# Optimization experiments

Hardware: AMD Instinct MI355X
Metric: run time of the kernel (lower is better)

## Reference

```python
import jax, jax.numpy as jnp
import numpy as np

H = 128  # hidden_dim
COORD_CLAMP = 100.0


def _glorot(key, shape):
    fan_in, fan_out = shape[0], shape[1]
    lim = float(np.sqrt(6.0 / (fan_in + fan_out)))
    return jax.random.uniform(key, shape, jnp.float32, -lim, lim)


def setup_inputs() -> dict:
    key = jax.random.key(0)
    ks = jax.random.split(key, 20)
    B, N = 2, 512
    inp = {
        "h": jax.random.normal(ks[0], (B, N, H), jnp.float32),
        "pos": jax.random.normal(ks[1], (B, N, 3), jnp.float32),
        "vel": jax.random.normal(ks[2], (B, N, 3), jnp.float32),
        # edge_mlp: Linear(2H+2 -> H), SiLU, Linear(H -> H), SiLU
        "We1": _glorot(ks[3], (2 * H + 2, H)), "be1": jnp.zeros((H,), jnp.float32),
        "We2": _glorot(ks[4], (H, H)), "be2": jnp.zeros((H,), jnp.float32),
        # attention_mlp: Linear(H -> 1), Sigmoid
        "Wa": _glorot(ks[5], (H, 1)), "ba": jnp.zeros((1,), jnp.float32),
        # pos_mlp: Linear(H -> H), SiLU, Linear(H -> 1, no bias)
        "Wp1": _glorot(ks[6], (H, H)), "bp1": jnp.zeros((H,), jnp.float32),
        "Wp2": _glorot(ks[7], (H, 1)),
        # vel_mlp: Linear(H -> H), SiLU, Linear(H -> 1, no bias)
        "Wv1": _glorot(ks[8], (H, H)), "bv1": jnp.zeros((H,), jnp.float32),
        "Wv2": _glorot(ks[9], (H, 1)),
        # node_mlp: Linear(2H -> H), SiLU, Linear(H -> H)
        "Wn1": _glorot(ks[10], (2 * H, H)), "bn1": jnp.zeros((H,), jnp.float32),
        "Wn2": _glorot(ks[11], (H, H)), "bn2": jnp.zeros((H,), jnp.float32),
    }
    return inp


def reference(h, pos, vel, We1, be1, We2, be2, Wa, ba,
              Wp1, bp1, Wp2, Wv1, bv1, Wv2, Wn1, bn1, Wn2, bn2):
    B, N, _ = pos.shape
    # pairwise diffs: [B, N, N, 3]
    pos_diff = pos[:, :, None, :] - pos[:, None, :, :]
    vel_diff = vel[:, :, None, :] - vel[:, None, :, :]
    pos_dist_sq = jnp.sum(pos_diff ** 2, axis=-1, keepdims=True)  # [B,N,N,1]
    vel_dist_sq = jnp.sum(vel_diff ** 2, axis=-1, keepdims=True)
    h_i = jnp.broadcast_to(h[:, :, None, :], (B, N, N, H))
    h_j = jnp.broadcast_to(h[:, None, :, :], (B, N, N, H))
    edge_input = jnp.concatenate([h_i, h_j, pos_dist_sq, vel_dist_sq], axis=-1)  # [B,N,N,2H+2]
    # edge MLP
    m = jax.nn.silu(jnp.einsum('bijc,ch->bijh', edge_input, We1) + be1)
    m_ij = jax.nn.silu(jnp.einsum('bijh,hk->bijk', m, We2) + be2)
    # attention gate
    att = jax.nn.sigmoid(jnp.einsum('bijh,ho->bijo', m_ij, Wa) + ba)  # [B,N,N,1]
    m_ij = m_ij * att
    # tanh-weighted coordinate/velocity updates
    pos_w = jnp.tanh(jnp.einsum('bijh,ho->bijo', jax.nn.silu(jnp.einsum('bijh,hk->bijk', m_ij, Wp1) + bp1), Wp2))
    vel_w = jnp.tanh(jnp.einsum('bijh,ho->bijo', jax.nn.silu(jnp.einsum('bijh,hk->bijk', m_ij, Wv1) + bv1), Wv2))
    denom = jnp.float32(max(N - 1, 1))
    pos_update = jnp.sum(pos_diff * pos_w, axis=2) / denom  # [B,N,3]
    vel_update = jnp.sum(vel_diff * vel_w, axis=2) / denom
    pos_out = jnp.clip(pos + pos_update, -COORD_CLAMP, COORD_CLAMP)
    vel_out = jnp.clip(vel + vel_update, -COORD_CLAMP, COORD_CLAMP)
    # node update
    m_agg = jnp.sum(m_ij, axis=2)  # [B,N,H]
    node_input = jnp.concatenate([h, m_agg], axis=-1)  # [B,N,2H]
    h_out = jax.nn.silu(jnp.einsum('bnc,ch->bnh', node_input, Wn1) + bn1)
    h_out = jnp.einsum('bnh,hk->bnk', h_out, Wn2) + bn2
    h_out = h + h_out  # residual
    return (h_out, pos_out, vel_out)
```

## Files before the change

kernel.cpp:

```cpp
#include <hip/hip_runtime.h>
#include <hip/hip_bf16.h>

#define Hd 128
#define Nn 512
#define TJ 32
#define LSTRIDE 136

typedef __bf16 bf16x8 __attribute__((ext_vector_type(8)));
typedef __bf16 bf16x4 __attribute__((ext_vector_type(4)));
typedef float  floatx4 __attribute__((ext_vector_type(4)));

__device__ __forceinline__ float frcp(float x){ return __builtin_amdgcn_rcpf(x); }
__device__ __forceinline__ float fsilu(float x){ return x * frcp(1.f + __expf(-x)); }
__device__ __forceinline__ float fsigm(float x){ return frcp(1.f + __expf(-x)); }
__device__ __forceinline__ float ftanh(float x){ return 1.f - 2.f * frcp(__expf(2.f*x) + 1.f); }
__device__ __forceinline__ float rfl(float x){
  return __int_as_float(__builtin_amdgcn_readfirstlane(__float_as_int(x)));
}

__global__ __launch_bounds__(256) void prep(const float* __restrict__ h,
                                            const float* __restrict__ We1,
                                            const float* __restrict__ be1,
                                            const float* __restrict__ We2,
                                            const float* __restrict__ Wp1,
                                            const float* __restrict__ Wv1,
                                            float* __restrict__ A,
                                            float* __restrict__ Bm,
                                            __bf16* __restrict__ dst,
                                            float* __restrict__ zbase){
  if (blockIdx.x < 256){
    const int r0 = blockIdx.x * 4;
    const int k = threadIdx.x & 127, ch = threadIdx.x >> 7;
    __shared__ float hL[4][Hd];
    __shared__ float pa[2][4][Hd], pb[2][4][Hd];
    for (int idx = threadIdx.x; idx < 4*Hd; idx += 256)
      hL[idx >> 7][idx & 127] = h[r0*Hd + idx];
    __syncthreads();
    float a[4] = {0.f,0.f,0.f,0.f}, bb[4] = {0.f,0.f,0.f,0.f};
    const int cbase = ch*64;
    #pragma unroll 4
    for (int cc = 0; cc < 64; ++cc){
      const int c = cbase + cc;
      const float wa = We1[c*Hd + k];
      const float wb = We1[(c + Hd)*Hd + k];
      #pragma unroll
      for (int rr = 0; rr < 4; ++rr){
        a[rr]  += hL[rr][c] * wa;
        bb[rr] += hL[rr][c] * wb;
      }
    }
    #pragma unroll
    for (int rr = 0; rr < 4; ++rr){ pa[ch][rr][k] = a[rr]; pb[ch][rr][k] = bb[rr]; }
    __syncthreads();
    if (threadIdx.x < Hd){
      const float be = be1[k];
      #pragma unroll
      for (int rr = 0; rr < 4; ++rr){
        A[(r0+rr)*Hd + k]  = pa[0][rr][k] + pa[1][rr][k] + be;
        Bm[(r0+rr)*Hd + k] = pb[0][rr][k] + pb[1][rr][k];
      }
    }
  } else if (blockIdx.x < 280){
    const int blk = blockIdx.x - 256;
    const int which = blk >> 3, m = blk & 7;
    const float* src = (which == 0) ? We2 : (which == 1 ? Wp1 : Wv1);
    __bf16* d = dst + which * (Hd*Hd);
    #pragma unroll
    for (int it = 0; it < 8; ++it){
      const int sidx = m*2048 + it*256 + threadIdx.x;
      const int kk = sidx >> 7, cc = sidx & 127;
      const int s = kk >> 5, j = kk & 7;
      const int lane = ((kk >> 3) & 3)*16 + (cc & 15);
      const int n = cc >> 4;
      d[n*2048 + s*512 + lane*8 + j] = (__bf16)src[sidx];
    }
  } else {
    const int t0 = (blockIdx.x - 280)*256 + threadIdx.x;
    for (int idx = t0; idx < 137216; idx += 2048) zbase[idx] = 0.f;
  }
}

__global__ __launch_bounds__(256) void egnn_bf(
    const float* __restrict__ pos, const float* __restrict__ vel,
    const float* __restrict__ We1, const float* __restrict__ be2,
    const float* __restrict__ Wa,  const float* __restrict__ ba,
    const float* __restrict__ bp1, const float* __restrict__ Wp2,
    const float* __restrict__ bv1, const float* __restrict__ Wv2,
    const float* __restrict__ A,   const float* __restrict__ Bm,
    const __bf16* __restrict__ Wsw,
    float* __restrict__ magg, float* __restrict__ posu, float* __restrict__ velu){

  const int t    = threadIdx.x;
  const int w    = t >> 6;
  const int lane = t & 63;
  const int q    = lane >> 4;
  const int l15  = lane & 15;
  const int node = blockIdx.x;
  const int b    = node >> 9;

  __shared__ float AiL[Hd], wpL[Hd], wvL[Hd];
  __shared__ float be2L[Hd], bp1L[Hd], bv1L[Hd], WaL[Hd], Wp2L[Hd], Wv2L[Hd];
  __shared__ __align__(16) __bf16 bufij[4*16*LSTRIDE];
  __shared__ float attW[4][16];
  __shared__ float sMag[4][Hd];
  __shared__ float sPV[4][6];

  if (t < Hd){
    AiL[t]  = A[(size_t)node*Hd + t];
    wpL[t]  = We1[256*Hd + t];
    wvL[t]  = We1[257*Hd + t];
    be2L[t] = be2[t]; bp1L[t] = bp1[t]; bv1L[t] = bv1[t];
    WaL[t]  = Wa[t];  Wp2L[t] = Wp2[t]; Wv2L[t] = Wv2[t];
  }
  const float baV = ba[0];
  const float* pi = &pos[(size_t)node*3];
  const float* vi = &vel[(size_t)node*3];
  const float px = rfl(pi[0]), py = rfl(pi[1]), pz = rfl(pi[2]);
  const float ux = rfl(vi[0]), uy = rfl(vi[1]), uz = rfl(vi[2]);
  __syncthreads();

  const bf16x8* We2s = (const bf16x8*)(Wsw);
  const bf16x8* Wp1s = (const bf16x8*)(Wsw + Hd*Hd);
  const bf16x8* Wv1s = (const bf16x8*)(Wsw + 2*Hd*Hd);
  __bf16* myBuf = &bufij[w*16*LSTRIDE];
  float*  myAtt = attW[w];

  float accP0=0.f, accP1=0.f, accP2=0.f, accV0=0.f, accV1=0.f, accV2=0.f;
  float acc8[8];
  #pragma unroll
  for (int e = 0; e < 8; ++e) acc8[e] = 0.f;

  for (int jt = 0; jt < 8; ++jt){
    const int j0 = w*128 + jt*16;
    const size_t row = (size_t)(b*Nn + j0 + l15);

    const float* pj = &pos[row*3];
    const float* vj = &vel[row*3];
    const float dx = px - pj[0], dy = py - pj[1], dz = pz - pj[2];
    const float dp = dx*dx + dy*dy + dz*dz;
    const float ex = ux - vj[0], ey = uy - vj[1], ez = uz - vj[2];
    const float dv = ex*ex + ey*ey + ez*ez;

    floatx4 acc[8];
    const floatx4 fzero = {0.f,0.f,0.f,0.f};
    #pragma unroll
    for (int fm = 0; fm < 8; ++fm) acc[fm] = fzero;

    #pragma unroll
    for (int s = 0; s < 4; ++s){
      const int fo = s*32 + q*8;
      const floatx4 A0 = *(const floatx4*)&AiL[fo], A1 = *(const floatx4*)&AiL[fo+4];
      const floatx4 P0 = *(const floatx4*)&wpL[fo], P1 = *(const floatx4*)&wpL[fo+4];
      const floatx4 V0 = *(const floatx4*)&wvL[fo], V1 = *(const floatx4*)&wvL[fo+4];
      const floatx4* Bp = (const floatx4*)&Bm[row*Hd + fo];
      const floatx4 b0 = Bp[0], b1 = Bp[1];
      float x[8];
      #pragma unroll
      for (int e = 0; e < 4; ++e){
        x[e]   = fsilu(A0[e] + b0[e] + dp*P0[e] + dv*V0[e]);
        x[4+e] = fsilu(A1[e] + b1[e] + dp*P1[e] + dv*V1[e]);
      }
      union { bf16x8 v; __hip_bfloat162 h2[4]; } o;
      o.h2[0] = __float22bfloat162_rn(make_float2(x[0], x[1]));
      o.h2[1] = __float22bfloat162_rn(make_float2(x[2], x[3]));
      o.h2[2] = __float22bfloat162_rn(make_float2(x[4], x[5]));
      o.h2[3] = __float22bfloat162_rn(make_float2(x[6], x[7]));
      #pragma unroll
      for (int fm = 0; fm < 8; ++fm){
        const bf16x8 a = We2s[(fm*4 + s)*64 + lane];
        acc[fm] = __builtin_amdgcn_mfma_f32_16x16x32_bf16(a, o.v, acc[fm], 0, 0, 0);
      }
    }

    float aw = 0.f;
    #pragma unroll
    for (int fm = 0; fm < 8; ++fm){
      const int fb = fm*16 + q*4;
      const floatx4 be = *(const floatx4*)&be2L[fb];
      const floatx4 wa = *(const floatx4*)&WaL[fb];
      float s0[4];
      #pragma unroll
      for (int r = 0; r < 4; ++r){
        s0[r] = fsilu(acc[fm][r] + be[r]);
        aw += s0[r]*wa[r];
      }
      union { bf16x4 v; __hip_bfloat162 h2[2]; } k0;
      k0.h2[0] = __float22bfloat162_rn(make_float2(s0[0], s0[1]));
      k0.h2[1] = __float22bfloat162_rn(make_float2(s0[2], s0[3]));
      *(bf16x4*)&myBuf[l15*LSTRIDE + fb] = k0.v;
    }
    aw += __shfl_xor(aw, 16, 64); aw += __shfl_xor(aw, 32, 64);
    const float att = fsigm(aw + baV);
    if (lane < 16) myAtt[l15] = att;

    #pragma unroll
    for (int fm = 0; fm < 8; ++fm) acc[fm] = fzero;
    #pragma unroll
    for (int s = 0; s < 4; ++s){
      const bf16x8 bfv = *(const bf16x8*)&myBuf[l15*LSTRIDE + s*32 + q*8];
      #pragma unroll
      for (int fm = 0; fm < 8; ++fm){
        const bf16x8 a = Wp1s[(fm*4 + s)*64 + lane];
        acc[fm] = __builtin_amdgcn_mfma_f32_16x16x32_bf16(a, bfv, acc[fm], 0, 0, 0);
      }
    }
    {
      float p = 0.f;
      #pragma unroll
      for (int fm = 0; fm < 8; ++fm){
        const int fb = fm*16 + q*4;
        const floatx4 bb = *(const floatx4*)&bp1L[fb];
        const floatx4 w2 = *(const floatx4*)&Wp2L[fb];
        #pragma unroll
        for (int r = 0; r < 4; ++r)
          p += fsilu(fmaf(att, acc[fm][r], bb[r])) * w2[r];
      }
      p += __shfl_xor(p, 16, 64); p += __shfl_xor(p, 32, 64);
      const float pw = ftanh(p);
      accP0 += (px - pj[0]) * pw;
      accP1 += (py - pj[1]) * pw;
      accP2 += (pz - pj[2]) * pw;
    }

    #pragma unroll
    for (int fm = 0; fm < 8; ++fm) acc[fm] = fzero;
    #pragma unroll
    for (int s = 0; s < 4; ++s){
      const bf16x8 bfv = *(const bf16x8*)&myBuf[l15*LSTRIDE + s*32 + q*8];
      #pragma unroll
      for (int fm = 0; fm < 8; ++fm){
        const bf16x8 a = Wv1s[(fm*4 + s)*64 + lane];
        acc[fm] = __builtin_amdgcn_mfma_f32_16x16x32_bf16(a, bfv, acc[fm], 0, 0, 0);
      }
    }
    {
      float p = 0.f;
      #pragma unroll
      for (int fm = 0; fm < 8; ++fm){
        const int fb = fm*16 + q*4;
        const floatx4 bb = *(const floatx4*)&bv1L[fb];
        const floatx4 w2 = *(const floatx4*)&Wv2L[fb];
        #pragma unroll
        for (int r = 0; r < 4; ++r)
          p += fsilu(fmaf(att, acc[fm][r], bb[r])) * w2[r];
      }
      p += __shfl_xor(p, 16, 64); p += __shfl_xor(p, 32, 64);
      const float vw = ftanh(p);
      accV0 += (ux - vj[0]) * vw;
      accV1 += (uy - vj[1]) * vw;
      accV2 += (uz - vj[2]) * vw;
    }

    {
      const int fg = lane & 15, jr = lane >> 4;
      #pragma unroll
      for (int k = 0; k < 4; ++k){
        const int jl = jr*4 + k;
        const float aj = myAtt[jl];
        const bf16x8 v = *(const bf16x8*)&myBuf[jl*LSTRIDE + fg*8];
        #pragma unroll
        for (int e = 0; e < 8; ++e) acc8[e] += aj * (float)v[e];
      }
    }
  }

  {
    float r6[6] = {accP0, accP1, accP2, accV0, accV1, accV2};
    #pragma unroll
    for (int off = 1; off < 64; off <<= 1){
      #pragma unroll
      for (int e = 0; e < 6; ++e) r6[e] += __shfl_xor(r6[e], off, 64);
    }
    if (lane == 0){
      #pragma unroll
      for (int e = 0; e < 6; ++e) sPV[w][e] = r6[e];
    }
    #pragma unroll
    for (int e = 0; e < 8; ++e){
      acc8[e] += __shfl_xor(acc8[e], 16, 64);
      acc8[e] += __shfl_xor(acc8[e], 32, 64);
    }
    if (lane < 16){
      *(float4*)&sMag[w][l15*8 + 0] = make_float4(acc8[0], acc8[1], acc8[2], acc8[3]);
      *(float4*)&sMag[w][l15*8 + 4] = make_float4(acc8[4], acc8[5], acc8[6], acc8[7]);
    }
  }
  __syncthreads();
  if (t < Hd){
    magg[(size_t)node*Hd + t] = sMag[0][t] + sMag[1][t] + sMag[2][t] + sMag[3][t];
  } else if (t < Hd + 3){
    const int d = t - Hd;
    posu[node*3 + d] = 0.25f*(sPV[0][d] + sPV[1][d] + sPV[2][d] + sPV[3][d]);
  } else if (t < Hd + 6){
    const int d = t - Hd - 3;
    velu[node*3 + d] = 0.25f*(sPV[0][3+d] + sPV[1][3+d] + sPV[2][3+d] + sPV[3][3+d]);
  }
}

__device__ __forceinline__ void gemm_kloopT(const __bf16* __restrict__ buf,
                                            const bf16x8* __restrict__ Ws,
                                            int w, int lane, int q, int l15,
                                            floatx4 acc[2][2]){
  const floatx4 zero = {0.f, 0.f, 0.f, 0.f};
  #pragma unroll
  for (int m = 0; m < 2; ++m){ acc[m][0] = zero; acc[m][1] = zero; }
  #pragma unroll
  for (int s = 0; s < 4; ++s){
    bf16x8 bf[2];
    #pragma unroll
    for (int n = 0; n < 2; ++n)
      bf[n] = *(const bf16x8*)&buf[(16*n + l15)*LSTRIDE + s*32 + q*8];
    const bf16x8 a0 = Ws[((2*w + 0)*4 + s)*64 + lane];
    const bf16x8 a1 = Ws[((2*w + 1)*4 + s)*64 + lane];
    #pragma unroll
    for (int n = 0; n < 2; ++n){
      acc[0][n] = __builtin_amdgcn_mfma_f32_16x16x32_bf16(a0, bf[n], acc[0][n], 0, 0, 0);
      acc[1][n] = __builtin_amdgcn_mfma_f32_16x16x32_bf16(a1, bf[n], acc[1][n], 0, 0, 0);
    }
  }
}

__device__ __forceinline__ void wdotT(floatx4 acc[2][2], float att0, float att1,
                                      const float* __restrict__ biasL,
                                      const float* __restrict__ w2L,
                                      int w, int lane, int q, int l15,
                                      float (*part)[TJ]){
  const int fb0 = 32*w + 4*q, fb1 = fb0 + 16;
  const floatx4 bb0 = *(const floatx4*)&biasL[fb0];
  const floatx4 bb1 = *(const floatx4*)&biasL[fb1];
  const floatx4 w0  = *(const floatx4*)&w2L[fb0];
  const floatx4 w1  = *(const floatx4*)&w2L[fb1];
  float p0 = 0.f, p1 = 0.f;
  #pragma unroll
  for (int r = 0; r < 4; ++r){
    p0 += fsilu(fmaf(att0, acc[0][0][r], bb0[r])) * w0[r];
    p0 += fsilu(fmaf(att0, acc[1][0][r], bb1[r])) * w1[r];
    p1 += fsilu(fmaf(att1, acc[0][1][r], bb0[r])) * w0[r];
    p1 += fsilu(fmaf(att1, acc[1][1][r], bb1[r])) * w1[r];
  }
  p0 += __shfl_xor(p0, 16, 64); p0 += __shfl_xor(p0, 32, 64);
  p1 += __shfl_xor(p1, 16, 64); p1 += __shfl_xor(p1, 32, 64);
  if (lane < 16){
    part[w][l15]      = p0;
    part[w][16 + l15] = p1;
  }
}

__global__ __launch_bounds__(256) void egnn_main(
    const float* __restrict__ pos, const float* __restrict__ vel,
    const float* __restrict__ We1, const float* __restrict__ be2,
    const float* __restrict__ Wa,  const float* __restrict__ ba,
    const float* __restrict__ bp1, const float* __restrict__ Wp2,
    const float* __restrict__ bv1, const float* __restrict__ Wv2,
    const float* __restrict__ A,   const float* __restrict__ Bm,
    const __bf16* __restrict__ Wsw,
    float* __restrict__ magg, float* __restrict__ posu, float* __restrict__ velu){

  const int t    = threadIdx.x;
  const int w    = t >> 6;
  const int lane = t & 63;
  const int q    = lane >> 4;
  const int l15  = lane & 15;
  const int node = blockIdx.x >> 1;
  const int half = blockIdx.x & 1;
  const int b    = node >> 9;

  __shared__ float AiL[Hd], wpL[Hd], wvL[Hd];
  __shared__ float be2L[Hd], bp1L[Hd], bv1L[Hd], WaL[Hd], Wp2L[Hd], Wv2L[Hd];
  __shared__ __align__(16) __bf16 bufm [TJ*LSTRIDE];
  __shared__ __align__(16) __bf16 bufij[TJ*LSTRIDE];
  __shared__ float partAtt[4][TJ], partP[4][TJ], partV[4][TJ];
  __shared__ float attL[TJ];

  if (t < Hd){
    AiL[t]  = A[node*Hd + t];
    wpL[t]  = We1[256*Hd + t];
    wvL[t]  = We1[257*Hd + t];
    be2L[t] = be2[t]; bp1L[t] = bp1[t]; bv1L[t] = bv1[t];
    WaL[t]  = Wa[t];  Wp2L[t] = Wp2[t]; Wv2L[t] = Wv2[t];
  }
  const float baV = ba[0];
  const float* pi = &pos[(size_t)node*3];
  const float* vi = &vel[(size_t)node*3];
  const float px = rfl(pi[0]), py = rfl(pi[1]), pz = rfl(pi[2]);
  const float ux = rfl(vi[0]), uy = rfl(vi[1]), uz = rfl(vi[2]);
  __syncthreads();

  const bf16x8* We2s = (const bf16x8*)(Wsw);
  const bf16x8* Wp1s = (const bf16x8*)(Wsw + Hd*Hd);
  const bf16x8* Wv1s = (const bf16x8*)(Wsw + 2*Hd*Hd);

  float accR[8];
  #pragma unroll
  for (int e = 0; e < 8; ++e) accR[e] = 0.f;

  for (int jt = 0; jt < (Nn/2)/TJ; ++jt){
    const int j0 = half*(Nn/2) + jt * TJ;
    {
      const int g  = t & 15;
      const int j2 = t >> 4;
      const floatx4 a0 = *(const floatx4*)&AiL[g*8];
      const floatx4 a1 = *(const floatx4*)&AiL[g*8 + 4];
      const floatx4 p0 = *(const floatx4*)&wpL[g*8];
      const floatx4 p1 = *(const floatx4*)&wpL[g*8 + 4];
      const floatx4 v0 = *(const floatx4*)&wvL[g*8];
      const floatx4 v1 = *(const floatx4*)&wvL[g*8 + 4];
      #pragma unroll
      for (int rr = 0; rr < 2; ++rr){
        const int j = j2 + rr*16;
        const int jg = j0 + j;
        const float* pj = &pos[(size_t)(b*Nn + jg)*3];
        const float* vj = &vel[(size_t)(b*Nn + jg)*3];
        const float dx = px - pj[0], dy = py - pj[1], dz = pz - pj[2];
        const float dp = dx*dx + dy*dy + dz*dz;
        const float ex = ux - vj[0], ey = uy - vj[1], ez = uz - vj[2];
        const float dv = ex*ex + ey*ey + ez*ez;
        const floatx4* Bp4 = (const floatx4*)&Bm[((size_t)(b*Nn + jg))*Hd + g*8];
        const floatx4 b0 = Bp4[0], b1 = Bp4[1];
        union { bf16x8 v; __hip_bfloat162 h2[4]; } o;
        float x[8];
        #pragma unroll
        for (int e = 0; e < 4; ++e){
          x[e]   = fsilu(a0[e] + b0[e] + dp*p0[e] + dv*v0[e]);
          x[4+e] = fsilu(a1[e] + b1[e] + dp*p1[e] + dv*v1[e]);
        }
        o.h2[0] = __float22bfloat162_rn(make_float2(x[0], x[1]));
        o.h2[1] = __float22bfloat162_rn(make_float2(x[2], x[3]));
        o.h2[2] = __float22bfloat162_rn(make_float2(x[4], x[5]));
        o.h2[3] = __float22bfloat162_rn(make_float2(x[6], x[7]));
        *(bf16x8*)&bufm[j*LSTRIDE + g*8] = o.v;
      }
    }
    __syncthreads();
    {
      floatx4 acc[2][2];
      gemm_kloopT(bufm, We2s, w, lane, q, l15, acc);
      const int fb0 = 32*w + 4*q, fb1 = fb0 + 16;
      const floatx4 be0 = *(const floatx4*)&be2L[fb0];
      const floatx4 be1v = *(const floatx4*)&be2L[fb1];
      const floatx4 wa0 = *(const floatx4*)&WaL[fb0];
      const floatx4 wa1 = *(const floatx4*)&WaL[fb1];
      float aw[2];
      #pragma unroll
      for (int n = 0; n < 2; ++n){
        const int j = 16*n + l15;
        float s0[4], s1[4];
        #pragma unroll
        for (int r = 0; r < 4; ++r){
          s0[r] = fsilu(acc[0][n][r] + be0[r]);
          s1[r] = fsilu(acc[1][n][r] + be1v[r]);
        }
        aw[n] = s0[0]*wa0[0] + s0[1]*wa0[1] + s0[2]*wa0[2] + s0[3]*wa0[3]
              + s1[0]*wa1[0] + s1[1]*wa1[1] + s1[2]*wa1[2] + s1[3]*wa1[3];
        union { bf16x4 v; __hip_bfloat162 h2[2]; } p0k, p1k;
        p0k.h2[0] = __float22bfloat162_rn(make_float2(s0[0], s0[1]));
        p0k.h2[1] = __float22bfloat162_rn(make_float2(s0[2], s0[3]));
        p1k.h2[0] = __float22bfloat162_rn(make_float2(s1[0], s1[1]));
        p1k.h2[1] = __float22bfloat162_rn(make_float2(s1[2], s1[3]));
        *(bf16x4*)&bufij[j*LSTRIDE + fb0] = p0k.v;
        *(bf16x4*)&bufij[j*LSTRIDE + fb1] = p1k.v;
      }
      aw[0] += __shfl_xor(aw[0], 16, 64); aw[0] += __shfl_xor(aw[0], 32, 64);
      aw[1] += __shfl_xor(aw[1], 16, 64); aw[1] += __shfl_xor(aw[1], 32, 64);
      if (lane < 16){
        partAtt[w][l15]      = aw[0];
        partAtt[w][16 + l15] = aw[1];
      }
    }
    __syncthreads();
    {
      const float att0 = fsigm(partAtt[0][l15] + partAtt[1][l15] +
                               partAtt[2][l15] + partAtt[3][l15] + baV);
      const float att1 = fsigm(partAtt[0][16+l15] + partAtt[1][16+l15] +
                               partAtt[2][16+l15] + partAtt[3][16+l15] + baV);
      if (w == 0 && lane < 16){ attL[l15] = att0; attL[16 + l15] = att1; }
      floatx4 acc[2][2];
      gemm_kloopT(bufij, Wp1s, w, lane, q, l15, acc);
      wdotT(acc, att0, att1, bp1L, Wp2L, w, lane, q, l15, partP);
      gemm_kloopT(bufij, Wv1s, w, lane, q, l15, acc);
      wdotT(acc, att0, att1, bv1L, Wv2L, w, lane, q, l15, partV);
    }
    __syncthreads();
    if (w == 0){
      if (lane < TJ){
        const int jg = j0 + lane;
        const float* pj = &pos[(size_t)(b*Nn + jg)*3];
        const float s4 = partP[0][lane] + partP[1][lane] + partP[2][lane] + partP[3][lane];
        const float pw = ftanh(s4);
        accR[0] += (px - pj[0]) * pw;
        accR[1] += (py - pj[1]) * pw;
        accR[2] += (pz - pj[2]) * pw;
      }
    } else if (w == 1){
      if (lane < TJ){
        const int jg = j0 + lane;
        const float* vj = &vel[(size_t)(b*Nn + jg)*3];
        const float s4 = partV[0][lane] + partV[1][lane] + partV[2][lane] + partV[3][lane];
        const float vw = ftanh(s4);
        accR[0] += (ux - vj[0]) * vw;
        accR[1] += (uy - vj[1]) * vw;
        accR[2] += (uz - vj[2]) * vw;
      }
    } else {
      const int sg   = (w - 2)*8 + (lane & 7);
      const int jsub = lane >> 3;
      #pragma unroll
      for (int jj = 0; jj < 4; ++jj){
        const int j = jj*8 + jsub;
        const float aj = attL[j];
        const bf16x8 v = *(const bf16x8*)&bufij[j*LSTRIDE + sg*8];
        #pragma unroll
        for (int e = 0; e < 8; ++e) accR[e] += aj * (float)v[e];
      }
    }
  }

  if (w == 0 || w == 1){
    float v0 = accR[0], v1 = accR[1], v2 = accR[2];
    #pragma unroll
    for (int off = 1; off < 64; off <<= 1){
      v0 += __shfl_xor(v0, off, 64);
      v1 += __shfl_xor(v1, off, 64);
      v2 += __shfl_xor(v2, off, 64);
    }
    if (lane == 0){
      float* dst = (w == 0) ? &posu[node*3] : &velu[node*3];
      atomicAdd(&dst[0], v0);
      atomicAdd(&dst[1], v1);
      atomicAdd(&dst[2], v2);
    }
  } else {
    const int sg = (w - 2)*8 + (lane & 7);
    #pragma unroll
    for (int off = 8; off < 64; off <<= 1){
      #pragma unroll
      for (int e = 0; e < 8; ++e) accR[e] += __shfl_xor(accR[e], off, 64);
    }
    if ((lane >> 3) == 0){
      #pragma unroll
      for (int e = 0; e < 8; ++e)
        atomicAdd(&magg[node*Hd + sg*8 + e], accR[e]);
    }
  }
}

__global__ __launch_bounds__(256) void egnn_final(
    const float* __restrict__ h, const float* __restrict__ pos, const float* __restrict__ vel,
    const float* __restrict__ Wn1, const float* __restrict__ bn1,
    const float* __restrict__ Wn2, const float* __restrict__ bn2,
    const float* __restrict__ magg, const float* __restrict__ posu,
    const float* __restrict__ velu, float* __restrict__ out){
  const int row = blockIdx.x;
  const int t = threadIdx.x;
  const int k = t & 127, ch = t >> 7;
  __shared__ float ni[2*Hd];
  __shared__ float p1[2][Hd], t1[Hd];
  ni[t] = (t < Hd) ? h[row*Hd + t] : magg[row*Hd + (t - Hd)];
  __syncthreads();
  {
    float a0=0.f,a1=0.f,a2=0.f,a3=0.f;
    const int cb = ch*Hd;
    #pragma unroll 8
    for (int cc = 0; cc < Hd; cc += 4){
      a0 += ni[cb+cc+0] * Wn1[(cb+cc+0)*Hd + k];
      a1 += ni[cb+cc+1] * Wn1[(cb+cc+1)*Hd + k];
      a2 += ni[cb+cc+2] * Wn1[(cb+cc+2)*Hd + k];
      a3 += ni[cb+cc+3] * Wn1[(cb+cc+3)*Hd + k];
    }
    p1[ch][k] = (a0+a1)+(a2+a3);
  }
  __syncthreads();
  if (t < Hd) t1[t] = fsilu(p1[0][t] + p1[1][t] + bn1[t]);
  __syncthreads();
  {
    float a0=0.f,a1=0.f,a2=0.f,a3=0.f;
    const int cb = ch*64;
    #pragma unroll 8
    for (int cc = 0; cc < 64; cc += 4){
      a0 += t1[cb+cc+0] * Wn2[(cb+cc+0)*Hd + k];
      a1 += t1[cb+cc+1] * Wn2[(cb+cc+1)*Hd + k];
      a2 += t1[cb+cc+2] * Wn2[(cb+cc+2)*Hd + k];
      a3 += t1[cb+cc+3] * Wn2[(cb+cc+3)*Hd + k];
    }
    p1[ch][k] = (a0+a1)+(a2+a3);
  }
  __syncthreads();
  if (t < Hd){
    out[row*Hd + t] = ni[t] + p1[0][t] + p1[1][t] + bn2[t];
  } else if (t < Hd + 3){
    const int d = t - Hd;
    const float v = pos[row*3 + d] + posu[row*3 + d] * (1.f/511.f);
    out[2*Nn*Hd + row*3 + d] = fminf(fmaxf(v, -100.f), 100.f);
  } else if (t < Hd + 6){
    const int d = t - Hd - 3;
    const float v = vel[row*3 + d] + velu[row*3 + d] * (1.f/511.f);
    out[2*Nn*Hd + 2*Nn*3 + row*3 + d] = fminf(fmaxf(v, -100.f), 100.f);
  }
}

extern "C" void kernel_launch(void* const* d_in, const int* in_sizes, int n_in,
                              void* d_out, int out_size, void* d_ws, size_t ws_size,
                              hipStream_t stream){
  const float* h   = (const float*)d_in[0];
  const float* pos = (const float*)d_in[1];
  const float* vel = (const float*)d_in[2];
  const float* We1 = (const float*)d_in[3];
  const float* be1 = (const float*)d_in[4];
  const float* We2 = (const float*)d_in[5];
  const float* be2 = (const float*)d_in[6];
  const float* Wa  = (const float*)d_in[7];
  const float* ba  = (const float*)d_in[8];
  const float* Wp1 = (const float*)d_in[9];
  const float* bp1 = (const float*)d_in[10];
  const float* Wp2 = (const float*)d_in[11];
  const float* Wv1 = (const float*)d_in[12];
  const float* bv1 = (const float*)d_in[13];
  const float* Wv2 = (const float*)d_in[14];
  const float* Wn1 = (const float*)d_in[15];
  const float* bn1 = (const float*)d_in[16];
  const float* Wn2 = (const float*)d_in[17];
  const float* bn2 = (const float*)d_in[18];

  float* ws = (float*)d_ws;
  float*  A    = ws;
  float*  Bmm  = ws + 131072;
  float*  magg = ws + 262144;
  float*  posu = ws + 393216;
  float*  velu = ws + 396288;
  __bf16* Wsw  = (__bf16*)(ws + 399360);
  float*  outp = (float*)d_out;

  hipFuncAttributes attr{};
  hipError_t ae = hipFuncGetAttributes(&attr, (const void*)egnn_bf);
  const bool useBf = (ae == hipSuccess && attr.numRegs > 0 && attr.numRegs <= 128);

  prep<<<dim3(288), dim3(256), 0, stream>>>(h, We1, be1, We2, Wp1, Wv1,
                                            A, Bmm, Wsw, magg);
  if (useBf){
    egnn_bf<<<dim3(1024), dim3(256), 0, stream>>>(pos, vel, We1, be2, Wa, ba, bp1, Wp2,
                                                  bv1, Wv2, A, Bmm, Wsw, magg, posu, velu);
  } else {
    egnn_main<<<dim3(2048), dim3(256), 0, stream>>>(pos, vel, We1, be2, Wa, ba, bp1, Wp2,
                                                    bv1, Wv2, A, Bmm, Wsw, magg, posu, velu);
  }
  egnn_final<<<dim3(1024), dim3(256), 0, stream>>>(h, pos, vel, Wn1, bn1, Wn2, bn2,
                                                   magg, posu, velu, outp);
}
```

Measured before the change: 234.5 us.

## Fuse node MLP into edge kernel and process 32 neighbors per wave iteration

The edge kernel now handles two 16-row neighbor tiles per loop iteration, so each loaded weight fragment feeds two MFMAs and weight loads per neighbor are halved. The final node MLP, residual, and pos/vel clamp are fused into the tail of the edge kernel, which removes the egnn_final launch and the magg/posu/velu round trip through global memory. The cost is higher register pressure (two accumulator sets plus cached activations) and a doubled LDS buffer, which may lower occupancy or push registers past the 128 threshold. If that threshold is exceeded, the fallback path is taken instead.

```diff
diff --git a/kernel.cpp b/kernel.cpp
--- a/kernel.cpp
+++ b/kernel.cpp
@@ -81,14 +81,17 @@
 }
 
 __global__ __launch_bounds__(256) void egnn_bf(
+    const float* __restrict__ h,
     const float* __restrict__ pos, const float* __restrict__ vel,
     const float* __restrict__ We1, const float* __restrict__ be2,
     const float* __restrict__ Wa,  const float* __restrict__ ba,
     const float* __restrict__ bp1, const float* __restrict__ Wp2,
     const float* __restrict__ bv1, const float* __restrict__ Wv2,
+    const float* __restrict__ Wn1, const float* __restrict__ bn1,
+    const float* __restrict__ Wn2, const float* __restrict__ bn2,
     const float* __restrict__ A,   const float* __restrict__ Bm,
     const __bf16* __restrict__ Wsw,
-    float* __restrict__ magg, float* __restrict__ posu, float* __restrict__ velu){
+    float* __restrict__ out){
 
   const int t    = threadIdx.x;
   const int w    = t >> 6;
@@ -100,10 +103,8 @@
 
   __shared__ float AiL[Hd], wpL[Hd], wvL[Hd];
   __shared__ float be2L[Hd], bp1L[Hd], bv1L[Hd], WaL[Hd], Wp2L[Hd], Wv2L[Hd];
-  __shared__ __align__(16) __bf16 bufij[4*16*LSTRIDE];
-  __shared__ float attW[4][16];
-  __shared__ float sMag[4][Hd];
-  __shared__ float sPV[4][6];
+  __shared__ __align__(16) __bf16 bufij[4*32*LSTRIDE];
+  __shared__ float attW[4][32];
 
   if (t < Hd){
     AiL[t]  = A[(size_t)node*Hd + t];
@@ -122,7 +123,7 @@
   const bf16x8* We2s = (const bf16x8*)(Wsw);
   const bf16x8* Wp1s = (const bf16x8*)(Wsw + Hd*Hd);
   const bf16x8* Wv1s = (const bf16x8*)(Wsw + 2*Hd*Hd);
-  __bf16* myBuf = &bufij[w*16*LSTRIDE];
+  __bf16* myBuf = &bufij[w*32*LSTRIDE];
   float*  myAtt = attW[w];
 
   float accP0=0.f, accP1=0.f, accP2=0.f, accV0=0.f, accV1=0.f, accV2=0.f;
@@ -130,132 +131,182 @@
   #pragma unroll
   for (int e = 0; e < 8; ++e) acc8[e] = 0.f;
 
-  for (int jt = 0; jt < 8; ++jt){
-    const int j0 = w*128 + jt*16;
-    const size_t row = (size_t)(b*Nn + j0 + l15);
-
-    const float* pj = &pos[row*3];
-    const float* vj = &vel[row*3];
-    const float dx = px - pj[0], dy = py - pj[1], dz = pz - pj[2];
-    const float dp = dx*dx + dy*dy + dz*dz;
-    const float ex = ux - vj[0], ey = uy - vj[1], ez = uz - vj[2];
-    const float dv = ex*ex + ey*ey + ez*ez;
-
-    floatx4 acc[8];
-    const floatx4 fzero = {0.f,0.f,0.f,0.f};
-    #pragma unroll
-    for (int fm = 0; fm < 8; ++fm) acc[fm] = fzero;
-
+  const floatx4 fzero = {0.f,0.f,0.f,0.f};
+
+  #pragma unroll 1
+  for (int jt = 0; jt < 4; ++jt){
+    const int j0 = w*128 + jt*32;
+    const size_t row0 = (size_t)(b*Nn + j0 + l15);
+    const size_t row1 = row0 + 16;
+
+    float dp[2], dv[2];
+    {
+      const float* pj0 = &pos[row0*3]; const float* vj0 = &vel[row0*3];
+      const float* pj1 = &pos[row1*3]; const float* vj1 = &vel[row1*3];
+      float dx = px - pj0[0], dy = py - pj0[1], dz = pz - pj0[2];
+      dp[0] = dx*dx + dy*dy + dz*dz;
+      dx = px - pj1[0]; dy = py - pj1[1]; dz = pz - pj1[2];
+      dp[1] = dx*dx + dy*dy + dz*dz;
+      float ex = ux - vj0[0], ey = uy - vj0[1], ez = uz - vj0[2];
+      dv[0] = ex*ex + ey*ey + ez*ez;
+      ex = ux - vj1[0]; ey = uy - vj1[1]; ez = uz - vj1[2];
+      dv[1] = ex*ex + ey*ey + ez*ez;
+    }
+
+    bf16x8 mf[4][2];
     #pragma unroll
     for (int s = 0; s < 4; ++s){
       const int fo = s*32 + q*8;
       const floatx4 A0 = *(const floatx4*)&AiL[fo], A1 = *(const floatx4*)&AiL[fo+4];
       const floatx4 P0 = *(const floatx4*)&wpL[fo], P1 = *(const floatx4*)&wpL[fo+4];
       const floatx4 V0 = *(const floatx4*)&wvL[fo], V1 = *(const floatx4*)&wvL[fo+4];
-      const floatx4* Bp = (const floatx4*)&Bm[row*Hd + fo];
-      const floatx4 b0 = Bp[0], b1 = Bp[1];
-      float x[8];
-      #pragma unroll
-      for (int e = 0; e < 4; ++e){
-        x[e]   = fsilu(A0[e] + b0[e] + dp*P0[e] + dv*V0[e]);
-        x[4+e] = fsilu(A1[e] + b1[e] + dp*P1[e] + dv*V1[e]);
-      }
-      union { bf16x8 v; __hip_bfloat162 h2[4]; } o;
-      o.h2[0] = __float22bfloat162_rn(make_float2(x[0], x[1]));
-      o.h2[1] = __float22bfloat162_rn(make_float2(x[2], x[3]));
-      o.h2[2] = __float22bfloat162_rn(make_float2(x[4], x[5]));
-      o.h2[3] = __float22bfloat162_rn(make_float2(x[6], x[7]));
-      #pragma unroll
-      for (int fm = 0; fm < 8; ++fm){
-        const bf16x8 a = We2s[(fm*4 + s)*64 + lane];
-        acc[fm] = __builtin_amdgcn_mfma_f32_16x16x32_bf16(a, o.v, acc[fm], 0, 0, 0);
-      }
-    }
-
-    float aw = 0.f;
-    #pragma unroll
-    for (int fm = 0; fm < 8; ++fm){
-      const int fb = fm*16 + q*4;
-      const floatx4 be = *(const floatx4*)&be2L[fb];
-      const floatx4 wa = *(const floatx4*)&WaL[fb];
-      float s0[4];
-      #pragma unroll
-      for (int r = 0; r < 4; ++r){
-        s0[r] = fsilu(acc[fm][r] + be[r]);
-        aw += s0[r]*wa[r];
-      }
-      union { bf16x4 v; __hip_bfloat162 h2[2]; } k0;
-      k0.h2[0] = __float22bfloat162_rn(make_float2(s0[0], s0[1]));
-      k0.h2[1] = __float22bfloat162_rn(make_float2(s0[2], s0[3]));
-      *(bf16x4*)&myBuf[l15*LSTRIDE + fb] = k0.v;
-    }
-    aw += __shfl_xor(aw, 16, 64); aw += __shfl_xor(aw, 32, 64);
-    const float att = fsigm(aw + baV);
-    if (lane < 16) myAtt[l15] = att;
-
-    #pragma unroll
-    for (int fm = 0; fm < 8; ++fm) acc[fm] = fzero;
-    #pragma unroll
-    for (int s = 0; s < 4; ++s){
-      const bf16x8 bfv = *(const bf16x8*)&myBuf[l15*LSTRIDE + s*32 + q*8];
-      #pragma unroll
-      for (int fm = 0; fm < 8; ++fm){
-        const bf16x8 a = Wp1s[(fm*4 + s)*64 + lane];
-        acc[fm] = __builtin_amdgcn_mfma_f32_16x16x32_bf16(a, bfv, acc[fm], 0, 0, 0);
-      }
-    }
+      #pragma unroll
+      for (int n = 0; n < 2; ++n){
+        const floatx4* Bp = (const floatx4*)&Bm[(n ? row1 : row0)*Hd + fo];
+        const floatx4 b0 = Bp[0], b1 = Bp[1];
+        float x[8];
+        #pragma unroll
+        for (int e = 0; e < 4; ++e){
+          x[e]   = fsilu(A0[e] + b0[e] + dp[n]*P0[e] + dv[n]*V0[e]);
+          x[4+e] = fsilu(A1[e] + b1[e] + dp[n]*P1[e] + dv[n]*V1[e]);
+        }
+        union { bf16x8 v; __hip_bfloat162 h2[4]; } o;
+        o.h2[0] = __float22bfloat162_rn(make_float2(x[0], x[1]));
+        o.h2[1] = __float22bfloat162_rn(make_float2(x[2], x[3]));
+        o.h2[2] = __float22bfloat162_rn(make_float2(x[4], x[5]));
+        o.h2[3] = __float22bfloat162_rn(make_float2(x[6], x[7]));
+        mf[s][n] = o.v;
+      }
+    }
+
+    float aw0 = 0.f, aw1 = 0.f;
+    #pragma unroll
+    for (int f = 0; f < 2; ++f){
+      floatx4 acc[4][2];
+      #pragma unroll
+      for (int m4 = 0; m4 < 4; ++m4){ acc[m4][0] = fzero; acc[m4][1] = fzero; }
+      #pragma unroll
+      for (int s = 0; s < 4; ++s){
+        #pragma unroll
+        for (int m4 = 0; m4 < 4; ++m4){
+          const bf16x8 a = We2s[((f*4 + m4)*4 + s)*64 + lane];
+          acc[m4][0] = __builtin_amdgcn_mfma_f32_16x16x32_bf16(a, mf[s][0], acc[m4][0], 0, 0, 0);
+          acc[m4][1] = __builtin_amdgcn_mfma_f32_16x16x32_bf16(a, mf[s][1], acc[m4][1], 0, 0, 0);
+        }
+      }
+      #pragma unroll
+      for (int m4 = 0; m4 < 4; ++m4){
+        const int fb = (f*4 + m4)*16 + q*4;
+        const floatx4 be = *(const floatx4*)&be2L[fb];
+        const floatx4 wa = *(const floatx4*)&WaL[fb];
+        float s0[4], s1[4];
+        #pragma unroll
+        for (int r = 0; r < 4; ++r){
+          s0[r] = fsilu(acc[m4][0][r] + be[r]);
+          s1[r] = fsilu(acc[m4][1][r] + be[r]);
+          aw0 += s0[r]*wa[r];
+          aw1 += s1[r]*wa[r];
+        }
+        union { bf16x4 v; __hip_bfloat162 h2[2]; } k0, k1;
+        k0.h2[0] = __float22bfloat162_rn(make_float2(s0[0], s0[1]));
+        k0.h2[1] = __float22bfloat162_rn(make_float2(s0[2], s0[3]));
+        k1.h2[0] = __float22bfloat162_rn(make_float2(s1[0], s1[1]));
+        k1.h2[1] = __float22bfloat162_rn(make_float2(s1[2], s1[3]));
+        *(bf16x4*)&myBuf[l15*LSTRIDE + fb]        = k0.v;
+        *(bf16x4*)&myBuf[(16 + l15)*LSTRIDE + fb] = k1.v;
+      }
+    }
+    aw0 += __shfl_xor(aw0, 16, 64); aw0 += __shfl_xor(aw0, 32, 64);
+    aw1 += __shfl_xor(aw1, 16, 64); aw1 += __shfl_xor(aw1, 32, 64);
+    const float att0 = fsigm(aw0 + baV);
+    const float att1 = fsigm(aw1 + baV);
+    if (lane < 16){ myAtt[l15] = att0; myAtt[16 + l15] = att1; }
+
     {
-      float p = 0.f;
-      #pragma unroll
-      for (int fm = 0; fm < 8; ++fm){
-        const int fb = fm*16 + q*4;
-        const floatx4 bb = *(const floatx4*)&bp1L[fb];
-        const floatx4 w2 = *(const floatx4*)&Wp2L[fb];
-        #pragma unroll
-        for (int r = 0; r < 4; ++r)
-          p += fsilu(fmaf(att, acc[fm][r], bb[r])) * w2[r];
-      }
-      p += __shfl_xor(p, 16, 64); p += __shfl_xor(p, 32, 64);
-      const float pw = ftanh(p);
-      accP0 += (px - pj[0]) * pw;
-      accP1 += (py - pj[1]) * pw;
-      accP2 += (pz - pj[2]) * pw;
-    }
-
-    #pragma unroll
-    for (int fm = 0; fm < 8; ++fm) acc[fm] = fzero;
-    #pragma unroll
-    for (int s = 0; s < 4; ++s){
-      const bf16x8 bfv = *(const bf16x8*)&myBuf[l15*LSTRIDE + s*32 + q*8];
-      #pragma unroll
-      for (int fm = 0; fm < 8; ++fm){
-        const bf16x8 a = Wv1s[(fm*4 + s)*64 + lane];
-        acc[fm] = __builtin_amdgcn_mfma_f32_16x16x32_bf16(a, bfv, acc[fm], 0, 0, 0);
-      }
-    }
+      float p0 = 0.f, p1 = 0.f;
+      #pragma unroll
+      for (int f = 0; f < 2; ++f){
+        floatx4 acc[4][2];
+        #pragma unroll
+        for (int m4 = 0; m4 < 4; ++m4){ acc[m4][0] = fzero; acc[m4][1] = fzero; }
+        #pragma unroll
+        for (int s = 0; s < 4; ++s){
+          const bf16x8 b0 = *(const bf16x8*)&myBuf[l15*LSTRIDE + s*32 + q*8];
+          const bf16x8 b1 = *(const bf16x8*)&myBuf[(16 + l15)*LSTRIDE + s*32 + q*8];
+          #pragma unroll
+          for (int m4 = 0; m4 < 4; ++m4){
+            const bf16x8 a = Wp1s[((f*4 + m4)*4 + s)*64 + lane];
+            acc[m4][0] = __builtin_amdgcn_mfma_f32_16x16x32_bf16(a, b0, acc[m4][0], 0, 0, 0);
+            acc[m4][1] = __builtin_amdgcn_mfma_f32_16x16x32_bf16(a, b1, acc[m4][1], 0, 0, 0);
+          }
+        }
+        #pragma unroll
+        for (int m4 = 0; m4 < 4; ++m4){
+          const int fb = (f*4 + m4)*16 + q*4;
+          const floatx4 bb = *(const floatx4*)&bp1L[fb];
+          const floatx4 w2 = *(const floatx4*)&Wp2L[fb];
+          #pragma unroll
+          for (int r = 0; r < 4; ++r){
+            p0 += fsilu(fmaf(att0, acc[m4][0][r], bb[r])) * w2[r];
+            p1 += fsilu(fmaf(att1, acc[m4][1][r], bb[r])) * w2[r];
+          }
+        }
+      }
+      p0 += __shfl_xor(p0, 16, 64); p0 += __shfl_xor(p0, 32, 64);
+      p1 += __shfl_xor(p1, 16, 64); p1 += __shfl_xor(p1, 32, 64);
+      const float pw0 = ftanh(p0), pw1 = ftanh(p1);
+      const float* pj0 = &pos[row0*3];
+      const float* pj1 = &pos[row1*3];
+      accP0 += (px - pj0[0])*pw0 + (px - pj1[0])*pw1;
+      accP1 += (py - pj0[1])*pw0 + (py - pj1[1])*pw1;
+      accP2 += (pz - pj0[2])*pw0 + (pz - pj1[2])*pw1;
+    }
+
     {
-      float p = 0.f;
-      #pragma unroll
-      for (int fm = 0; fm < 8; ++fm){
-        const int fb = fm*16 + q*4;
-        const floatx4 bb = *(const floatx4*)&bv1L[fb];
-        const floatx4 w2 = *(const floatx4*)&Wv2L[fb];
-        #pragma unroll
-        for (int r = 0; r < 4; ++r)
-          p += fsilu(fmaf(att, acc[fm][r], bb[r])) * w2[r];
-      }
-      p += __shfl_xor(p, 16, 64); p += __shfl_xor(p, 32, 64);
-      const float vw = ftanh(p);
-      accV0 += (ux - vj[0]) * vw;
-      accV1 += (uy - vj[1]) * vw;
-      accV2 += (uz - vj[2]) * vw;
+      float p0 = 0.f, p1 = 0.f;
+      #pragma unroll
+      for (int f = 0; f < 2; ++f){
+        floatx4 acc[4][2];
+        #pragma unroll
+        for (int m4 = 0; m4 < 4; ++m4){ acc[m4][0] = fzero; acc[m4][1] = fzero; }
+        #pragma unroll
+        for (int s = 0; s < 4; ++s){
+          const bf16x8 b0 = *(const bf16x8*)&myBuf[l15*LSTRIDE + s*32 + q*8];
+          const bf16x8 b1 = *(const bf16x8*)&myBuf[(16 + l15)*LSTRIDE + s*32 + q*8];
+          #pragma unroll
+          for (int m4 = 0; m4 < 4; ++m4){
+            const bf16x8 a = Wv1s[((f*4 + m4)*4 + s)*64 + lane];
+            acc[m4][0] = __builtin_amdgcn_mfma_f32_16x16x32_bf16(a, b0, acc[m4][0], 0, 0, 0);
+            acc[m4][1] = __builtin_amdgcn_mfma_f32_16x16x32_bf16(a, b1, acc[m4][1], 0, 0, 0);
+          }
+        }
+        #pragma unroll
+        for (int m4 = 0; m4 < 4; ++m4){
+          const int fb = (f*4 + m4)*16 + q*4;
+          const floatx4 bb = *(const floatx4*)&bv1L[fb];
+          const floatx4 w2 = *(const floatx4*)&Wv2L[fb];
+          #pragma unroll
+          for (int r = 0; r < 4; ++r){
+            p0 += fsilu(fmaf(att0, acc[m4][0][r], bb[r])) * w2[r];
+            p1 += fsilu(fmaf(att1, acc[m4][1][r], bb[r])) * w2[r];
+          }
+        }
+      }
+      p0 += __shfl_xor(p0, 16, 64); p0 += __shfl_xor(p0, 32, 64);
+      p1 += __shfl_xor(p1, 16, 64); p1 += __shfl_xor(p1, 32, 64);
+      const float vw0 = ftanh(p0), vw1 = ftanh(p1);
+      const float* vj0 = &vel[row0*3];
+      const float* vj1 = &vel[row1*3];
+      accV0 += (ux - vj0[0])*vw0 + (ux - vj1[0])*vw1;
+      accV1 += (uy - vj0[1])*vw0 + (uy - vj1[1])*vw1;
+      accV2 += (uz - vj0[2])*vw0 + (uz - vj1[2])*vw1;
     }
 
     {
       const int fg = lane & 15, jr = lane >> 4;
       #pragma unroll
-      for (int k = 0; k < 4; ++k){
-        const int jl = jr*4 + k;
+      for (int k = 0; k < 8; ++k){
+        const int jl = jr*8 + k;
         const float aj = myAtt[jl];
         const bf16x8 v = *(const bf16x8*)&myBuf[jl*LSTRIDE + fg*8];
         #pragma unroll
@@ -264,6 +315,8 @@
     }
   }
 
+  float* sMagW = (float*)myBuf;
+  float* sPVW  = (float*)myBuf + 128;
   {
     float r6[6] = {accP0, accP1, accP2, accV0, accV1, accV2};
     #pragma unroll
@@ -273,7 +326,7 @@
     }
     if (lane == 0){
       #pragma unroll
-      for (int e = 0; e < 6; ++e) sPV[w][e] = r6[e];
+      for (int e = 0; e < 6; ++e) sPVW[e] = r6[e];
     }
     #pragma unroll
     for (int e = 0; e < 8; ++e){
@@ -281,20 +334,66 @@
       acc8[e] += __shfl_xor(acc8[e], 32, 64);
     }
     if (lane < 16){
-      *(float4*)&sMag[w][l15*8 + 0] = make_float4(acc8[0], acc8[1], acc8[2], acc8[3]);
-      *(float4*)&sMag[w][l15*8 + 4] = make_float4(acc8[4], acc8[5], acc8[6], acc8[7]);
-    }
-  }
-  __syncthreads();
-  if (t < Hd){
-    magg[(size_t)node*Hd + t] = sMag[0][t] + sMag[1][t] + sMag[2][t] + sMag[3][t];
-  } else if (t < Hd + 3){
-    const int d = t - Hd;
-    posu[node*3 + d] = 0.25f*(sPV[0][d] + sPV[1][d] + sPV[2][d] + sPV[3][d]);
-  } else if (t < Hd + 6){
-    const int d = t - Hd - 3;
-    velu[node*3 + d] = 0.25f*(sPV[0][3+d] + sPV[1][3+d] + sPV[2][3+d] + sPV[3][3+d]);
-  }
+      *(float4*)&sMagW[l15*8 + 0] = make_float4(acc8[0], acc8[1], acc8[2], acc8[3]);
+      *(float4*)&sMagW[l15*8 + 4] = make_float4(acc8[4], acc8[5], acc8[6], acc8[7]);
+    }
+  }
+  __syncthreads();
+
+  float* sF = (float*)bufij + 1024;
+  {
+    const float* s0 = (const float*)(bufij);
+    const float* s1 = (const float*)(bufij + 32*LSTRIDE);
+    const float* s2 = (const float*)(bufij + 64*LSTRIDE);
+    const float* s3 = (const float*)(bufij + 96*LSTRIDE);
+    if (t < Hd){
+      sF[128 + t] = s0[t] + s1[t] + s2[t] + s3[t];
+      sF[t] = h[(size_t)node*Hd + t];
+    } else if (t < Hd + 3){
+      const int d = t - Hd;
+      const float v = 0.25f*(s0[128+d] + s1[128+d] + s2[128+d] + s3[128+d]);
+      const float o = pi[d] + v*(1.f/511.f);
+      out[2*Nn*Hd + node*3 + d] = fminf(fmaxf(o, -100.f), 100.f);
+    } else if (t < Hd + 6){
+      const int d = t - Hd - 3;
+      const float v = 0.25f*(s0[131+d] + s1[131+d] + s2[131+d] + s3[131+d]);
+      const float o = vi[d] + v*(1.f/511.f);
+      out[2*Nn*Hd + 2*Nn*3 + node*3 + d] = fminf(fmaxf(o, -100.f), 100.f);
+    }
+  }
+  __syncthreads();
+  {
+    const int k = t & 127, ch = t >> 7;
+    const int cb = ch*Hd;
+    float a0=0.f,a1=0.f,a2=0.f,a3=0.f;
+    #pragma unroll 8
+    for (int cc = 0; cc < Hd; cc += 4){
+      a0 += sF[cb+cc+0] * Wn1[(cb+cc+0)*Hd + k];
+      a1 += sF[cb+cc+1] * Wn1[(cb+cc+1)*Hd + k];
+      a2 += sF[cb+cc+2] * Wn1[(cb+cc+2)*Hd + k];
+      a3 += sF[cb+cc+3] * Wn1[(cb+cc+3)*Hd + k];
+    }
+    sF[256 + ch*128 + k] = (a0+a1)+(a2+a3);
+  }
+  __syncthreads();
+  if (t < Hd) sF[512 + t] = fsilu(sF[256 + t] + sF[384 + t] + bn1[t]);
+  __syncthreads();
+  {
+    const int k = t & 127, ch = t >> 7;
+    const int cb = ch*64;
+    float a0=0.f,a1=0.f,a2=0.f,a3=0.f;
+    #pragma unroll 8
+    for (int cc = 0; cc < 64; cc += 4){
+      a0 += sF[512+cb+cc+0] * Wn2[(cb+cc+0)*Hd + k];
+      a1 += sF[512+cb+cc+1] * Wn2[(cb+cc+1)*Hd + k];
+      a2 += sF[512+cb+cc+2] * Wn2[(cb+cc+2)*Hd + k];
+      a3 += sF[512+cb+cc+3] * Wn2[(cb+cc+3)*Hd + k];
+    }
+    sF[256 + ch*128 + k] = (a0+a1)+(a2+a3);
+  }
+  __syncthreads();
+  if (t < Hd)
+    out[(size_t)node*Hd + t] = sF[t] + sF[256 + t] + sF[384 + t] + bn2[t];
 }
 
 __device__ __forceinline__ void gemm_kloopT(const __bf16* __restrict__ buf,
@@ -637,12 +736,13 @@
   prep<<<dim3(288), dim3(256), 0, stream>>>(h, We1, be1, We2, Wp1, Wv1,
                                             A, Bmm, Wsw, magg);
   if (useBf){
-    egnn_bf<<<dim3(1024), dim3(256), 0, stream>>>(pos, vel, We1, be2, Wa, ba, bp1, Wp2,
-                                                  bv1, Wv2, A, Bmm, Wsw, magg, posu, velu);
+    egnn_bf<<<dim3(1024), dim3(256), 0, stream>>>(h, pos, vel, We1, be2, Wa, ba,
+                                                  bp1, Wp2, bv1, Wv2, Wn1, bn1,
+                                                  Wn2, bn2, A, Bmm, Wsw, outp);
   } else {
     egnn_main<<<dim3(2048), dim3(256), 0, stream>>>(pos, vel, We1, be2, Wa, ba, bp1, Wp2,
                                                     bv1, Wv2, A, Bmm, Wsw, magg, posu, velu);
-  }
-  egnn_final<<<dim3(1024), dim3(256), 0, stream>>>(h, pos, vel, Wn1, bn1, Wn2, bn2,
-                                                   magg, posu, velu, outp);
+    egnn_final<<<dim3(1024), dim3(256), 0, stream>>>(h, pos, vel, Wn1, bn1, Wn2, bn2,
+                                                     magg, posu, velu, outp);
+  }
 }
```

New measurement: 235.1 us. About the same (+0.3%).
